# Performance work log

Measured on AMD Instinct MI355X. Metric: run time of the kernel, lower is better.

Reference implementation:

```python
import jax, jax.numpy as jnp
import numpy as np

B, S, D = 256, 512, 64
LN_EPS = 1e-5


def _layernorm(x, g, b):
    mu = jnp.mean(x, axis=-1, keepdims=True)
    var = jnp.mean(jnp.square(x - mu), axis=-1, keepdims=True)
    return (x - mu) * jax.lax.rsqrt(var + LN_EPS) * g + b


def _mha(xq, xkv, in_w, in_b, out_w, out_b):
    # in_w: (3D, D) packed [Wq; Wk; Wv] as in torch nn.MultiheadAttention
    wq, wk, wv = in_w[:D], in_w[D:2 * D], in_w[2 * D:]
    bq, bk, bv = in_b[:D], in_b[D:2 * D], in_b[2 * D:]
    q = xq @ wq.T + bq      # (B, Sq, D)
    k = xkv @ wk.T + bk     # (B, Sk, D)
    v = xkv @ wv.T + bv
    scores = jnp.einsum('bqd,bkd->bqk', q, k) / jnp.sqrt(jnp.asarray(D, q.dtype))
    attn = jax.nn.softmax(scores, axis=-1)
    out = jnp.einsum('bqk,bkd->bqd', attn, v)
    return out @ out_w.T + out_b


def setup_inputs() -> dict:
    key = jax.random.key(0)
    ks = jax.random.split(key, 14)
    s = 1.0 / np.sqrt(D)
    return {
        'x_src': jax.random.normal(ks[0], (B, S), jnp.float32),
        'x_tgt': jax.random.normal(ks[1], (B, S), jnp.float32),
        'proj_w': jax.random.normal(ks[2], (D,), jnp.float32) * s,   # Linear(1, D) weight squeezed
        'proj_b': jax.random.normal(ks[3], (D,), jnp.float32) * 0.02,
        'sa_in_w': jax.random.normal(ks[4], (3 * D, D), jnp.float32) * s,
        'sa_in_b': jnp.zeros((3 * D,), jnp.float32),
        'sa_out_w': jax.random.normal(ks[5], (D, D), jnp.float32) * s,
        'sa_out_b': jnp.zeros((D,), jnp.float32),
        'sa_ln_g': jnp.ones((D,), jnp.float32),
        'sa_ln_b': jnp.zeros((D,), jnp.float32),
        'ca_in_w': jax.random.normal(ks[6], (3 * D, D), jnp.float32) * s,
        'ca_in_b': jnp.zeros((3 * D,), jnp.float32),
        'ca_out_w': jax.random.normal(ks[7], (D, D), jnp.float32) * s,
        'ca_out_b': jnp.zeros((D,), jnp.float32),
        'ca_ln_g': jnp.ones((D,), jnp.float32),
        'ca_ln_b': jnp.zeros((D,), jnp.float32),
    }


def reference(x_src, x_tgt, proj_w, proj_b,
              sa_in_w, sa_in_b, sa_out_w, sa_out_b, sa_ln_g, sa_ln_b,
              ca_in_w, ca_in_b, ca_out_w, ca_out_b, ca_ln_g, ca_ln_b):
    # Input projection: (B, S) -> (B, S, D) via Linear(1, D)
    hs = x_src[..., None] * proj_w + proj_b
    ht = x_tgt[..., None] * proj_w + proj_b
    # Shared self-attention block (pre-residual + LayerNorm), then mean pool
    zs = _layernorm(hs + _mha(hs, hs, sa_in_w, sa_in_b, sa_out_w, sa_out_b), sa_ln_g, sa_ln_b)
    zt = _layernorm(ht + _mha(ht, ht, sa_in_w, sa_in_b, sa_out_w, sa_out_b), sa_ln_g, sa_ln_b)
    z_src_private = zs.mean(axis=1)
    z_tgt_private = zt.mean(axis=1)
    # Cross-attention: Q from source, K/V from target
    zc = _layernorm(hs + _mha(hs, ht, ca_in_w, ca_in_b, ca_out_w, ca_out_b), ca_ln_g, ca_ln_b)
    z_shared = zc.mean(axis=1)
    return (z_shared, z_src_private, z_tgt_private)
```

## Files before the change

### kernel.cpp

```cpp
#include <hip/hip_runtime.h>

#define BB 256
#define SS 512
#define DD 64
#define LN_EPS 1e-5f
#define L2E 1.4426950408889634f

#define WS_TYPE_STRIDE 256

typedef float v2f __attribute__((ext_vector_type(2)));

__device__ __forceinline__ float fexp2(float x) {
#if __has_builtin(__builtin_amdgcn_exp2f)
    return __builtin_amdgcn_exp2f(x);
#else
    float r; asm("v_exp_f32 %0, %1" : "=v"(r) : "v"(x)); return r;
#endif
}

__global__ __launch_bounds__(1024) void prep_kernel(
    const float* __restrict__ proj_w, const float* __restrict__ proj_b,
    const float* __restrict__ sa_in_w, const float* __restrict__ sa_in_b,
    const float* __restrict__ sa_out_w, const float* __restrict__ sa_out_b,
    const float* __restrict__ ca_in_w, const float* __restrict__ ca_in_b,
    const float* __restrict__ ca_out_w, const float* __restrict__ ca_out_b,
    float* __restrict__ ws)
{
    const int tid = threadIdx.x;
    __shared__ float sv[2][6][DD];
    __shared__ float suu[2][DD], see[2][DD];

    if (tid < 768) {
        const int mat = tid >> 6, d = tid & 63;
        const int type = mat / 6, which = mat % 6;
        const int rb = which % 3;
        const int vecsel = which / 3;
        const float* W = (type ? ca_in_w : sa_in_w) + (rb * DD + d) * DD;
        const float* v = vecsel ? proj_b : proj_w;
        float s = 0.f;
        #pragma unroll
        for (int e = 0; e < DD; e += 4) {
            float4 wv = *(const float4*)(W + e);
            float4 vv = *(const float4*)(v + e);
            s += wv.x * vv.x + wv.y * vv.y + wv.z * vv.z + wv.w * vv.w;
        }
        if (vecsel) s += (type ? ca_in_b : sa_in_b)[rb * DD + d];
        sv[type][which][d] = s;
    }
    __syncthreads();

    if (tid < 256) {
        const int mat = tid >> 6, d = tid & 63;
        const int type = mat >> 1, which = mat & 1;
        const float* W = (type ? ca_out_w : sa_out_w) + d * DD;
        const float* v = sv[type][which ? 5 : 2];
        float s = 0.f;
        #pragma unroll
        for (int e = 0; e < DD; e += 4) {
            float4 wv = *(const float4*)(W + e);
            s += wv.x * v[e] + wv.y * v[e + 1] + wv.z * v[e + 2] + wv.w * v[e + 3];
        }
        if (which) {
            s += (type ? ca_out_b : sa_out_b)[d];
            see[type][d] = proj_b[d] + s;
        } else {
            suu[type][d] = s;
        }
    }
    __syncthreads();

    const int wave = tid >> 6, lane = tid & 63;
    if (wave < 2) {
        const int type = wave;
        auto wred = [](float x) {
            #pragma unroll
            for (int o = 32; o > 0; o >>= 1) x += __shfl_down(x, o);
            return __shfl(x, 0);
        };
        const float aq = sv[type][0][lane], ak = sv[type][1][lane];
        const float cq = sv[type][3][lane];
        const float pw = proj_w[lane];
        const float u  = suu[type][lane], e = see[type][lane];

        const float alpha = wred(aq * ak) * 0.125f;
        const float gamma = wred(cq * ak) * 0.125f;
        const float m_pw = wred(pw) * (1.f / DD);
        const float m_u  = wred(u)  * (1.f / DD);
        const float m_e  = wred(e)  * (1.f / DD);
        const float a  = pw - m_pw;
        const float bb = u  - m_u;
        const float c  = e  - m_e;
        const float G11 = wred(a * a)   * (1.f / DD);
        const float G22 = wred(bb * bb) * (1.f / DD);
        const float G33 = wred(c * c)   * (1.f / DD);
        const float G12 = wred(a * bb)  * (1.f / DD);
        const float G13 = wred(a * c)   * (1.f / DD);
        const float G23 = wred(bb * c)  * (1.f / DD);

        float* w = ws + type * WS_TYPE_STRIDE;
        w[8 + lane] = a; w[72 + lane] = bb; w[136 + lane] = c;
        if (lane == 0) {
            w[0] = alpha; w[1] = gamma;
            w[2] = G11; w[3] = G22; w[4] = G33; w[5] = G12; w[6] = G13; w[7] = G23;
        }
    }
}

__global__ __launch_bounds__(512) void attn_kernel(
    const float* __restrict__ x_src, const float* __restrict__ x_tgt,
    const float* __restrict__ sa_ln_g, const float* __restrict__ sa_ln_b,
    const float* __restrict__ ca_ln_g, const float* __restrict__ ca_ln_b,
    const float* __restrict__ ws, float* __restrict__ out)
{
    const int tid  = threadIdx.x;
    const int b    = blockIdx.x / 3;
    const int task = blockIdx.x % 3;
    const float* xq_g = (task == 1) ? (x_tgt + b * SS) : (x_src + b * SS);
    const float* y_g  = (task == 0) ? (x_src + b * SS) : (x_tgt + b * SS);
    const int type    = (task == 2) ? 1 : 0;
    const float* w  = ws + type * WS_TYPE_STRIDE;
    const float* g  = type ? ca_ln_g : sa_ln_g;
    const float* lb = type ? ca_ln_b : sa_ln_b;
    const int out_base = ((task == 0) ? BB * DD : (task == 1) ? 2 * BB * DD : 0) + b * DD;

    __shared__ __align__(16) float ys_l[SS];
    __shared__ float rmax[8], rmin[8], rP[8], rT[8], rI[8];
    __shared__ float bc[5];

    const int wave = tid >> 6, lane = tid & 63;

    const float xq = xq_g[tid];
    const float y  = y_g[tid];
    ys_l[tid] = y;

    float mymax = y, mymin = y;
    #pragma unroll
    for (int o = 32; o > 0; o >>= 1) {
        mymax = fmaxf(mymax, __shfl_down(mymax, o));
        mymin = fminf(mymin, __shfl_down(mymin, o));
    }
    if (lane == 0) { rmax[wave] = mymax; rmin[wave] = mymin; }
    __syncthreads();
    if (tid == 0) {
        float a = rmax[0], bmn = rmin[0];
        #pragma unroll
        for (int i = 1; i < 8; ++i) { a = fmaxf(a, rmax[i]); bmn = fminf(bmn, rmin[i]); }
        bc[0] = a; bc[1] = bmn;
    }
    __syncthreads();
    const float ymax = bc[0], ymin = bc[1];

    const float alpha = w[0], gamma = w[1];
    const float G11 = w[2], G22 = w[3], G33 = w[4], G12 = w[5], G13 = w[6], G23 = w[7];

    const float c   = alpha * xq + gamma;
    const float clf = c * L2E;
    const float nml = -fmaxf(c * ymax, c * ymin) * L2E;
    const v2f cl  = { clf, clf };
    const v2f nm  = { nml, nml };

    v2f den = { 0.f, 0.f }, num = { 0.f, 0.f };
    #pragma unroll 4
    for (int k = 0; k < SS; k += 8) {
        float4 ya = *(const float4*)&ys_l[k];
        float4 yb = *(const float4*)&ys_l[k + 4];
        v2f y0 = { ya.x, ya.y }, y1 = { ya.z, ya.w };
        v2f y2 = { yb.x, yb.y }, y3 = { yb.z, yb.w };
        v2f a0 = cl * y0 + nm;
        v2f a1 = cl * y1 + nm;
        v2f a2 = cl * y2 + nm;
        v2f a3 = cl * y3 + nm;
        v2f E0 = { fexp2(a0.x), fexp2(a0.y) };
        v2f E1 = { fexp2(a1.x), fexp2(a1.y) };
        v2f E2 = { fexp2(a2.x), fexp2(a2.y) };
        v2f E3 = { fexp2(a3.x), fexp2(a3.y) };
        den += E0; num += y0 * E0;
        den += E1; num += y1 * E1;
        den += E2; num += y2 * E2;
        den += E3; num += y3 * E3;
    }
    const float t = (num.x + num.y) / (den.x + den.y);

    const float var = xq * xq * G11 + t * t * G22 + G33
                    + 2.f * (xq * t * G12 + xq * G13 + t * G23);
    const float inv = rsqrtf(var + LN_EPS);

    float pP = xq * inv, pT = t * inv, pI = inv;
    #pragma unroll
    for (int o = 32; o > 0; o >>= 1) {
        pP += __shfl_down(pP, o);
        pT += __shfl_down(pT, o);
        pI += __shfl_down(pI, o);
    }
    if (lane == 0) { rP[wave] = pP; rT[wave] = pT; rI[wave] = pI; }
    __syncthreads();
    if (tid == 0) {
        float sP = 0.f, sT = 0.f, sI = 0.f;
        #pragma unroll
        for (int i = 0; i < 8; ++i) { sP += rP[i]; sT += rT[i]; sI += rI[i]; }
        bc[2] = sP * (1.f / SS); bc[3] = sT * (1.f / SS); bc[4] = sI * (1.f / SS);
    }
    __syncthreads();

    if (tid < DD) {
        const float P = bc[2], T = bc[3], I = bc[4];
        float z = (P * w[8 + tid] + T * w[72 + tid] + I * w[136 + tid]) * g[tid] + lb[tid];
        out[out_base + tid] = z;
    }
}

extern "C" void kernel_launch(void* const* d_in, const int* in_sizes, int n_in,
                              void* d_out, int out_size, void* d_ws, size_t ws_size,
                              hipStream_t stream) {
    const float* x_src    = (const float*)d_in[0];
    const float* x_tgt    = (const float*)d_in[1];
    const float* proj_w   = (const float*)d_in[2];
    const float* proj_b   = (const float*)d_in[3];
    const float* sa_in_w  = (const float*)d_in[4];
    const float* sa_in_b  = (const float*)d_in[5];
    const float* sa_out_w = (const float*)d_in[6];
    const float* sa_out_b = (const float*)d_in[7];
    const float* sa_ln_g  = (const float*)d_in[8];
    const float* sa_ln_b  = (const float*)d_in[9];
    const float* ca_in_w  = (const float*)d_in[10];
    const float* ca_in_b  = (const float*)d_in[11];
    const float* ca_out_w = (const float*)d_in[12];
    const float* ca_out_b = (const float*)d_in[13];
    const float* ca_ln_g  = (const float*)d_in[14];
    const float* ca_ln_b  = (const float*)d_in[15];
    float* ws  = (float*)d_ws;
    float* out = (float*)d_out;

    prep_kernel<<<1, 1024, 0, stream>>>(proj_w, proj_b,
                                        sa_in_w, sa_in_b, sa_out_w, sa_out_b,
                                        ca_in_w, ca_in_b, ca_out_w, ca_out_b, ws);
    attn_kernel<<<BB * 3, 512, 0, stream>>>(x_src, x_tgt,
                                            sa_ln_g, sa_ln_b, ca_ln_g, ca_ln_b,
                                            ws, out);
}
```

Measured before the change: 118.2 us.

## Fuse weight-prep kernel into attention kernel, recomputing constants per block

Merges the single-block prep kernel into the per-batch attention kernel. Each block now recomputes its own projected vectors, Gram terms and softmax constants in shared memory instead of reading them from a workspace. This removes one kernel launch and the serial dependency on a one-block prep kernel. In exchange, every one of the 768 blocks redoes small matrix-vector products over the 64x64 weights and adds barrier-separated phases before the exp loop.

```diff
diff --git a/kernel.cpp b/kernel.cpp
--- a/kernel.cpp
+++ b/kernel.cpp
@@ -5,8 +5,6 @@
 #define DD 64
 #define LN_EPS 1e-5f
 #define L2E 1.4426950408889634f
-
-#define WS_TYPE_STRIDE 256
 
 typedef float v2f __attribute__((ext_vector_type(2)));
 
@@ -18,24 +16,58 @@
 #endif
 }
 
-__global__ __launch_bounds__(1024) void prep_kernel(
+__global__ __launch_bounds__(512, 6) void fused_kernel(
+    const float* __restrict__ x_src, const float* __restrict__ x_tgt,
     const float* __restrict__ proj_w, const float* __restrict__ proj_b,
     const float* __restrict__ sa_in_w, const float* __restrict__ sa_in_b,
     const float* __restrict__ sa_out_w, const float* __restrict__ sa_out_b,
+    const float* __restrict__ sa_ln_g, const float* __restrict__ sa_ln_b,
     const float* __restrict__ ca_in_w, const float* __restrict__ ca_in_b,
     const float* __restrict__ ca_out_w, const float* __restrict__ ca_out_b,
-    float* __restrict__ ws)
+    const float* __restrict__ ca_ln_g, const float* __restrict__ ca_ln_b,
+    float* __restrict__ out)
 {
-    const int tid = threadIdx.x;
-    __shared__ float sv[2][6][DD];
-    __shared__ float suu[2][DD], see[2][DD];
-
-    if (tid < 768) {
+    const int tid  = threadIdx.x;
+    const int b    = blockIdx.x / 3;
+    const int task = blockIdx.x % 3;
+    const float* xq_g = (task == 1) ? (x_tgt + b * SS) : (x_src + b * SS);
+    const float* y_g  = (task == 0) ? (x_src + b * SS) : (x_tgt + b * SS);
+    const int type    = (task == 2) ? 1 : 0;
+    const float* in_w  = type ? ca_in_w  : sa_in_w;
+    const float* in_b  = type ? ca_in_b  : sa_in_b;
+    const float* out_w = type ? ca_out_w : sa_out_w;
+    const float* out_b = type ? ca_out_b : sa_out_b;
+    const float* g     = type ? ca_ln_g  : sa_ln_g;
+    const float* lb    = type ? ca_ln_b  : sa_ln_b;
+    const int out_base = ((task == 0) ? BB * DD : (task == 1) ? 2 * BB * DD : 0) + b * DD;
+
+    __shared__ float sv[6][DD];
+    __shared__ float cvec[3][DD];
+    __shared__ float cst[8];
+    __shared__ __align__(16) float ys_l[SS];
+    __shared__ float rmax[8], rmin[8], rP[8], rT[8], rI[8];
+    __shared__ float bc[5];
+
+    const int wave = tid >> 6, lane = tid & 63;
+
+    const float xq = xq_g[tid];
+    const float y  = y_g[tid];
+    ys_l[tid] = y;
+
+    {
+        float mx = y, mn = y;
+        #pragma unroll
+        for (int o = 32; o > 0; o >>= 1) {
+            mx = fmaxf(mx, __shfl_down(mx, o));
+            mn = fminf(mn, __shfl_down(mn, o));
+        }
+        if (lane == 0) { rmax[wave] = mx; rmin[wave] = mn; }
+    }
+
+    if (tid < 384) {
         const int mat = tid >> 6, d = tid & 63;
-        const int type = mat / 6, which = mat % 6;
-        const int rb = which % 3;
-        const int vecsel = which / 3;
-        const float* W = (type ? ca_in_w : sa_in_w) + (rb * DD + d) * DD;
+        const int rb = mat % 3, vecsel = mat / 3;
+        const float* W = in_w + (rb * DD + d) * DD;
         const float* v = vecsel ? proj_b : proj_w;
         float s = 0.f;
         #pragma unroll
@@ -44,43 +76,41 @@
             float4 vv = *(const float4*)(v + e);
             s += wv.x * vv.x + wv.y * vv.y + wv.z * vv.z + wv.w * vv.w;
         }
-        if (vecsel) s += (type ? ca_in_b : sa_in_b)[rb * DD + d];
-        sv[type][which][d] = s;
-    }
-    __syncthreads();
-
-    if (tid < 256) {
-        const int mat = tid >> 6, d = tid & 63;
-        const int type = mat >> 1, which = mat & 1;
-        const float* W = (type ? ca_out_w : sa_out_w) + d * DD;
-        const float* v = sv[type][which ? 5 : 2];
+        if (vecsel) s += in_b[rb * DD + d];
+        sv[mat][d] = s;
+    }
+    __syncthreads();
+
+    if (tid < 128) {
+        const int which = tid >> 6, d = tid & 63;
+        const float* W = out_w + d * DD;
+        const float* v = sv[which ? 5 : 2];
         float s = 0.f;
         #pragma unroll
         for (int e = 0; e < DD; e += 4) {
             float4 wv = *(const float4*)(W + e);
             s += wv.x * v[e] + wv.y * v[e + 1] + wv.z * v[e + 2] + wv.w * v[e + 3];
         }
-        if (which) {
-            s += (type ? ca_out_b : sa_out_b)[d];
-            see[type][d] = proj_b[d] + s;
-        } else {
-            suu[type][d] = s;
-        }
-    }
-    __syncthreads();
-
-    const int wave = tid >> 6, lane = tid & 63;
-    if (wave < 2) {
-        const int type = wave;
+        if (which) cvec[2][d] = proj_b[d] + s + out_b[d];
+        else       cvec[1][d] = s;
+    }
+    if (tid == 511) {
+        float a = rmax[0], m = rmin[0];
+        #pragma unroll
+        for (int i = 1; i < 8; ++i) { a = fmaxf(a, rmax[i]); m = fminf(m, rmin[i]); }
+        bc[0] = a; bc[1] = m;
+    }
+    __syncthreads();
+
+    if (wave == 0) {
         auto wred = [](float x) {
             #pragma unroll
             for (int o = 32; o > 0; o >>= 1) x += __shfl_down(x, o);
             return __shfl(x, 0);
         };
-        const float aq = sv[type][0][lane], ak = sv[type][1][lane];
-        const float cq = sv[type][3][lane];
+        const float aq = sv[0][lane], ak = sv[1][lane], cq = sv[3][lane];
         const float pw = proj_w[lane];
-        const float u  = suu[type][lane], e = see[type][lane];
+        const float u  = cvec[1][lane], e = cvec[2][lane];
 
         const float alpha = wred(aq * ak) * 0.125f;
         const float gamma = wred(cq * ak) * 0.125f;
@@ -97,67 +127,25 @@
         const float G13 = wred(a * c)   * (1.f / DD);
         const float G23 = wred(bb * c)  * (1.f / DD);
 
-        float* w = ws + type * WS_TYPE_STRIDE;
-        w[8 + lane] = a; w[72 + lane] = bb; w[136 + lane] = c;
+        cvec[0][lane] = a; cvec[1][lane] = bb; cvec[2][lane] = c;
         if (lane == 0) {
-            w[0] = alpha; w[1] = gamma;
-            w[2] = G11; w[3] = G22; w[4] = G33; w[5] = G12; w[6] = G13; w[7] = G23;
-        }
-    }
-}
-
-__global__ __launch_bounds__(512) void attn_kernel(
-    const float* __restrict__ x_src, const float* __restrict__ x_tgt,
-    const float* __restrict__ sa_ln_g, const float* __restrict__ sa_ln_b,
-    const float* __restrict__ ca_ln_g, const float* __restrict__ ca_ln_b,
-    const float* __restrict__ ws, float* __restrict__ out)
-{
-    const int tid  = threadIdx.x;
-    const int b    = blockIdx.x / 3;
-    const int task = blockIdx.x % 3;
-    const float* xq_g = (task == 1) ? (x_tgt + b * SS) : (x_src + b * SS);
-    const float* y_g  = (task == 0) ? (x_src + b * SS) : (x_tgt + b * SS);
-    const int type    = (task == 2) ? 1 : 0;
-    const float* w  = ws + type * WS_TYPE_STRIDE;
-    const float* g  = type ? ca_ln_g : sa_ln_g;
-    const float* lb = type ? ca_ln_b : sa_ln_b;
-    const int out_base = ((task == 0) ? BB * DD : (task == 1) ? 2 * BB * DD : 0) + b * DD;
-
-    __shared__ __align__(16) float ys_l[SS];
-    __shared__ float rmax[8], rmin[8], rP[8], rT[8], rI[8];
-    __shared__ float bc[5];
-
-    const int wave = tid >> 6, lane = tid & 63;
-
-    const float xq = xq_g[tid];
-    const float y  = y_g[tid];
-    ys_l[tid] = y;
-
-    float mymax = y, mymin = y;
-    #pragma unroll
-    for (int o = 32; o > 0; o >>= 1) {
-        mymax = fmaxf(mymax, __shfl_down(mymax, o));
-        mymin = fminf(mymin, __shfl_down(mymin, o));
-    }
-    if (lane == 0) { rmax[wave] = mymax; rmin[wave] = mymin; }
-    __syncthreads();
-    if (tid == 0) {
-        float a = rmax[0], bmn = rmin[0];
-        #pragma unroll
-        for (int i = 1; i < 8; ++i) { a = fmaxf(a, rmax[i]); bmn = fminf(bmn, rmin[i]); }
-        bc[0] = a; bc[1] = bmn;
-    }
-    __syncthreads();
+            cst[0] = alpha; cst[1] = gamma;
+            cst[2] = G11; cst[3] = G22; cst[4] = G33;
+            cst[5] = G12; cst[6] = G13; cst[7] = G23;
+        }
+    }
+    __syncthreads();
+
     const float ymax = bc[0], ymin = bc[1];
-
-    const float alpha = w[0], gamma = w[1];
-    const float G11 = w[2], G22 = w[3], G33 = w[4], G12 = w[5], G13 = w[6], G23 = w[7];
+    const float alpha = cst[0], gamma = cst[1];
+    const float G11 = cst[2], G22 = cst[3], G33 = cst[4];
+    const float G12 = cst[5], G13 = cst[6], G23 = cst[7];
 
     const float c   = alpha * xq + gamma;
     const float clf = c * L2E;
     const float nml = -fmaxf(c * ymax, c * ymin) * L2E;
-    const v2f cl  = { clf, clf };
-    const v2f nm  = { nml, nml };
+    const v2f cl = { clf, clf };
+    const v2f nm = { nml, nml };
 
     v2f den = { 0.f, 0.f }, num = { 0.f, 0.f };
     #pragma unroll 4
@@ -204,7 +192,7 @@
 
     if (tid < DD) {
         const float P = bc[2], T = bc[3], I = bc[4];
-        float z = (P * w[8 + tid] + T * w[72 + tid] + I * w[136 + tid]) * g[tid] + lb[tid];
+        float z = (P * cvec[0][tid] + T * cvec[1][tid] + I * cvec[2][tid]) * g[tid] + lb[tid];
         out[out_base + tid] = z;
     }
 }
@@ -228,13 +216,11 @@
     const float* ca_out_b = (const float*)d_in[13];
     const float* ca_ln_g  = (const float*)d_in[14];
     const float* ca_ln_b  = (const float*)d_in[15];
-    float* ws  = (float*)d_ws;
     float* out = (float*)d_out;
 
-    prep_kernel<<<1, 1024, 0, stream>>>(proj_w, proj_b,
-                                        sa_in_w, sa_in_b, sa_out_w, sa_out_b,
-                                        ca_in_w, ca_in_b, ca_out_w, ca_out_b, ws);
-    attn_kernel<<<BB * 3, 512, 0, stream>>>(x_src, x_tgt,
-                                            sa_ln_g, sa_ln_b, ca_ln_g, ca_ln_b,
-                                            ws, out);
+    fused_kernel<<<BB * 3, 512, 0, stream>>>(
+        x_src, x_tgt, proj_w, proj_b,
+        sa_in_w, sa_in_b, sa_out_w, sa_out_b, sa_ln_g, sa_ln_b,
+        ca_in_w, ca_in_b, ca_out_w, ca_out_b, ca_ln_g, ca_ln_b,
+        out);
 }
```

Measured after the change: 119.8 us. About the same (+1.4%).
